# Performance work log

Measured on AMD Instinct MI355X. Metric: run time of the kernel, lower is better.

The kernel has to match this reference:

```python
import jax, jax.numpy as jnp
import numpy as np

HEADS = 4
OUT = 100   # = max_num_peds
IN = 100    # = max_num_peds
NEG_SLOPE = 0.2  # both GATConv attention leakyrelu (PyG default) and module's nn.LeakyReLU(0.2)


def setup_inputs() -> dict:
    key = jax.random.key(0)
    k0, k1, k2, k3 = jax.random.split(key, 4)
    A = jax.random.normal(k0, (1024, 100, 100), jnp.float32)
    # GATConv linear weight [heads*out, in] and attention vectors [heads, out]
    W = jax.random.normal(k1, (HEADS * OUT, IN), jnp.float32) * 0.1
    att_src = jax.random.normal(k2, (HEADS, OUT), jnp.float32) * 0.1
    att_dst = jax.random.normal(k3, (HEADS, OUT), jnp.float32) * 0.1
    bias = jnp.zeros((OUT,), jnp.float32)
    return {"A": A, "W": W, "att_src": att_src, "att_dst": att_dst, "bias": bias}


def reference(A, W, att_src, att_dst, bias):
    # A: [T, N, N] with N == max_num_peds, so the F.pad in the original is a no-op.
    T, _, N = A.shape
    X = jnp.swapaxes(A, 1, 2)                      # x = A_t.T for every t -> [T, N, IN]
    Wh = W.reshape(HEADS, OUT, IN)
    H = jnp.einsum('tnf,hof->tnho', X, Wh)         # per-head projected features [T,N,H,OUT]
    a_s = jnp.einsum('tnho,ho->tnh', H, att_src)   # source attention logits [T,N,H]
    a_d = jnp.einsum('tnho,ho->tnh', H, att_dst)   # dest attention logits   [T,N,H]
    # fully-connected graph + self loops (PyG add_self_loops=True) -> dense [T, i, j, H]
    logits = jax.nn.leaky_relu(a_d[:, :, None, :] + a_s[:, None, :, :], NEG_SLOPE)
    alpha = jax.nn.softmax(logits, axis=2)         # softmax over source nodes j per dest i
    out = jnp.einsum('tijh,tjho->tiho', alpha, H)  # aggregate [T,N,H,OUT]
    out = out.mean(axis=2) + bias                  # concat=False -> mean over heads, + bias
    x = jax.nn.leaky_relu(out, NEG_SLOPE)          # module's self.lrelu
    new_A = jnp.swapaxes(x, 1, 2)[:, :N, :N] + jnp.eye(N, dtype=A.dtype)
    return new_A
```

## Files before the change

### kernel.cpp

```cpp
#include <hip/hip_runtime.h>
#include <hip/hip_bf16.h>

typedef __attribute__((ext_vector_type(8))) short bf16x8;
typedef __attribute__((ext_vector_type(4))) float f32x4;
typedef __attribute__((ext_vector_type(4))) unsigned u32x4;

#define NEG 0.2f
#define CST 104
#define HSTRIDE 11648
#define POFF 24192

__device__ __forceinline__ float lrelu(float x) { return x >= 0.0f ? x : NEG * x; }

__device__ __forceinline__ unsigned pk2(float a, float b) {
    __hip_bfloat162 h = __float22bfloat162_rn(float2{a, b});
    unsigned r;
    __builtin_memcpy(&r, &h, sizeof(r));
    return r;
}
__device__ __forceinline__ float bflo(unsigned u) {
    unsigned v = u << 16; float f; __builtin_memcpy(&f, &v, 4); return f;
}
__device__ __forceinline__ float bfhi(unsigned u) {
    unsigned v = u & 0xffff0000u; float f; __builtin_memcpy(&f, &v, 4); return f;
}

extern "C" __global__ void prep_w(const float* __restrict__ W,
                                  const float* __restrict__ att_src,
                                  const float* __restrict__ att_dst,
                                  unsigned short* __restrict__ Wp)
{
    __shared__ float red[2][4][128];
    __shared__ float sWS[128], sWD[128];
    const int h = blockIdx.x, tid = threadIdx.x;
    const int f = tid & 127, og = tid >> 7;
    const float* __restrict__ Wh = W + h * 10000;
    float ws = 0.0f, wd = 0.0f;
    if (f < 100) {
        for (int o = og * 25; o < og * 25 + 25; ++o) {
            float wv = Wh[o * 100 + f];
            ws = fmaf(att_src[h * 100 + o], wv, ws);
            wd = fmaf(att_dst[h * 100 + o], wv, wd);
        }
    }
    red[0][og][f] = ws;
    red[1][og][f] = wd;
    __syncthreads();
    if (tid < 256) {
        const int which = tid >> 7, ff = tid & 127;
        float s = (red[which][0][ff] + red[which][1][ff]) +
                  (red[which][2][ff] + red[which][3][ff]);
        (which ? sWD : sWS)[ff] = s;
    }
    __syncthreads();
    unsigned short* __restrict__ D = Wp + h * HSTRIDE;
    for (int q = tid; q < 2912; q += 512) {
        const int o = q / 26, f0 = (q - o * 26) * 4;
        uint2 pp = {0u, 0u};
        if (f0 < 100) {
            if (o < 100) {
                float4 wv = *(const float4*)(Wh + o * 100 + f0);
                pp.x = pk2(wv.x, wv.y);
                pp.y = pk2(wv.z, wv.w);
            } else if (o == 100) {
                pp.x = pk2(sWS[f0], sWS[f0 + 1]);
                pp.y = pk2(sWS[f0 + 2], sWS[f0 + 3]);
            } else if (o == 101) {
                pp.x = pk2(sWD[f0], sWD[f0 + 1]);
                pp.y = pk2(sWD[f0 + 2], sWD[f0 + 3]);
            }
        }
        *(uint2*)(D + o * CST + f0) = pp;
    }
}

extern "C" __global__ void __launch_bounds__(512, 4)
gat19(const float* __restrict__ A, const unsigned short* __restrict__ Wp,
      const float* __restrict__ bias, float* __restrict__ out)
{
    extern __shared__ char smem[];
    unsigned short* HT = (unsigned short*)smem;
    float* sas  = (float*)(smem + 23296);
    float* sad  = (float*)(smem + 23744);
    unsigned short* P  = (unsigned short*)(smem + POFF);
    float* sOut = (float*)smem;

    const int t    = blockIdx.x;
    const int tid  = threadIdx.x;
    const int w    = tid >> 6;
    const int l    = tid & 63;
    const int lr   = l & 15;
    const int lk   = l >> 4;
    const bool HASW = (w < 7);
    const int row  = HASW ? w : 6;
    const int j0   = row * 16 + 4 * lk;
    const bool JW  = HASW && (j0 < 104);
    const float* __restrict__ At = A + (size_t)t * 10000u;
    const f32x4 z4 = {0, 0, 0, 0};

    if (tid < 224) {
        float v = (tid >= 100 && tid < 112) ? -1e30f : 0.0f;
        ((float*)(smem + 23296))[tid] = v;
    }

    {
        const char* Wg = (const char*)Wp;
#pragma unroll
        for (int k = 0; k < 3; ++k) {
            const int c0 = k * 512 + w * 64;
            if (c0 < 1456)
                __builtin_amdgcn_global_load_lds(
                    (const __attribute__((address_space(1))) unsigned*)(Wg + c0 * 16 + l * 16),
                    (__attribute__((address_space(3))) unsigned*)(smem + POFF + c0 * 16),
                    16, 0, 0);
        }
    }

    const int col = row * 16 + lr;
    const bool cOK = HASW && (col < 100);
    bf16x8 xf[4];
#pragma unroll
    for (int ks = 0; ks < 4; ++ks) {
        const bool kill = (ks == 3) && (lk != 0);
        const int koff = ks * 32 + lk * 8;
        u32x4 uv = {0u, 0u, 0u, 0u};
        if (cOK && !kill) {
#pragma unroll
            for (int jp = 0; jp < 4; ++jp) {
                const int f0 = koff + jp * 2;
                float a0 = (f0     < 100) ? At[f0 * 100 + col]       : 0.0f;
                float a1 = (f0 + 1 < 100) ? At[(f0 + 1) * 100 + col] : 0.0f;
                uv[jp] = pk2(a0, a1);
            }
        }
        xf[ks] = __builtin_bit_cast(bf16x8, uv);
    }
    __syncthreads();

    f32x4 acc[7];
#pragma unroll
    for (int c = 0; c < 7; ++c) acc[c] = z4;

    for (int h = 0; h < 4; ++h) {
        if (HASW) {
#pragma unroll
            for (int half = 0; half < 2; ++half) {
                const int ntn = half ? 3 : 4;
                f32x4 c[4];
#pragma unroll
                for (int cc = 0; cc < 4; ++cc) c[cc] = z4;
                __builtin_amdgcn_s_setprio(1);
#pragma unroll
                for (int ks = 0; ks < 4; ++ks) {
                    const int koff = ks * 32 + lk * 8;
                    bf16x8 b[4];
#pragma unroll
                    for (int bb = 0; bb < 4; ++bb)
                        if (bb < ntn)
                            b[bb] = *(const bf16x8*)(P + ((half * 4 + bb) * 16 + lr) * CST + koff);
#pragma unroll
                    for (int bb = 0; bb < 4; ++bb)
                        if (bb < ntn)
                            c[bb] = __builtin_amdgcn_mfma_f32_16x16x32_bf16(xf[ks], b[bb], c[bb], 0, 0, 0);
                }
                __builtin_amdgcn_s_setprio(0);
#pragma unroll
                for (int bb = 0; bb < 4; ++bb)
                    if (bb < ntn) {
                        const int o = (half * 4 + bb) * 16 + lr;
                        if (JW) {
                            uint2 pp;
                            pp.x = pk2(c[bb].x, c[bb].y);
                            pp.y = pk2(c[bb].z, c[bb].w);
                            *(uint2*)(HT + o * CST + j0) = pp;
                        }
                    }
                if (half == 1) {
                    if (lr == 4 && j0 < 100) *(f32x4*)(sas + j0) = c[2];
                    if (lr == 5 && JW)       *(f32x4*)(sad + j0) = c[2];
                }
            }
        }
        __syncthreads();

        if (h < 3) {
            const char* Wg = (const char*)(Wp + (h + 1) * HSTRIDE);
#pragma unroll
            for (int k = 0; k < 3; ++k) {
                const int c0 = k * 512 + w * 64;
                if (c0 < 1456)
                    __builtin_amdgcn_global_load_lds(
                        (const __attribute__((address_space(1))) unsigned*)(Wg + c0 * 16 + l * 16),
                        (__attribute__((address_space(3))) unsigned*)(smem + POFF + c0 * 16),
                        16, 0, 0);
            }
        }

        if (HASW) {
            const float adi = sad[row * 16 + lr];
            float sE = 0.0f;
            bf16x8 af[4];
#pragma unroll
            for (int ks = 0; ks < 4; ++ks) {
                const bool dead = (ks == 3) && (lk != 0);
                const int jb = dead ? 64 : ks * 32 + lk * 8;
                const f32x4 s0 = *(const f32x4*)(sas + jb);
                const f32x4 s1 = *(const f32x4*)(sas + jb + 4);
                float e0 = dead ? 0.0f : __expf(lrelu(adi + s0.x));
                float e1 = dead ? 0.0f : __expf(lrelu(adi + s0.y));
                float e2 = dead ? 0.0f : __expf(lrelu(adi + s0.z));
                float e3 = dead ? 0.0f : __expf(lrelu(adi + s0.w));
                float e4 = dead ? 0.0f : __expf(lrelu(adi + s1.x));
                float e5 = dead ? 0.0f : __expf(lrelu(adi + s1.y));
                float e6 = dead ? 0.0f : __expf(lrelu(adi + s1.z));
                float e7 = dead ? 0.0f : __expf(lrelu(adi + s1.w));
                sE += ((e0 + e1) + (e2 + e3)) + ((e4 + e5) + (e6 + e7));
                u32x4 uv;
                uv.x = pk2(e0, e1); uv.y = pk2(e2, e3);
                uv.z = pk2(e4, e5); uv.w = pk2(e6, e7);
                af[ks] = __builtin_bit_cast(bf16x8, uv);
            }
            sE += __shfl_xor(sE, 16);
            sE += __shfl_xor(sE, 32);
            const float invE = sE > 0.0f ? __builtin_amdgcn_rcpf(sE) : 0.0f;
#pragma unroll
            for (int ks = 0; ks < 4; ++ks) {
                u32x4 uv = __builtin_bit_cast(u32x4, af[ks]);
                uv.x = pk2(bflo(uv.x) * invE, bfhi(uv.x) * invE);
                uv.y = pk2(bflo(uv.y) * invE, bfhi(uv.y) * invE);
                uv.z = pk2(bflo(uv.z) * invE, bfhi(uv.z) * invE);
                uv.w = pk2(bflo(uv.w) * invE, bfhi(uv.w) * invE);
                af[ks] = __builtin_bit_cast(bf16x8, uv);
            }

            __builtin_amdgcn_s_setprio(1);
#pragma unroll
            for (int half = 0; half < 2; ++half) {
                const int ntn = half ? 3 : 4;
#pragma unroll
                for (int ks = 0; ks < 4; ++ks) {
                    const int koff = ks * 32 + lk * 8;
                    bf16x8 b[4];
#pragma unroll
                    for (int bb = 0; bb < 4; ++bb)
                        if (bb < ntn)
                            b[bb] = *(const bf16x8*)(HT + ((half * 4 + bb) * 16 + lr) * CST + koff);
#pragma unroll
                    for (int bb = 0; bb < 4; ++bb)
                        if (bb < ntn)
                            acc[half * 4 + bb] = __builtin_amdgcn_mfma_f32_16x16x32_bf16(
                                af[ks], b[bb], acc[half * 4 + bb], 0, 0, 0);
                }
            }
            __builtin_amdgcn_s_setprio(0);
        }
        __syncthreads();
    }

    if (JW) {
        const int i0 = j0;
#pragma unroll
        for (int tn = 0; tn < 7; ++tn) {
            const int o = tn * 16 + lr;
            const float b = (o < 100) ? bias[o] : 0.0f;
            f32x4 v;
            v.x = lrelu(acc[tn].x * 0.25f + b) + ((i0 + 0) == o ? 1.0f : 0.0f);
            v.y = lrelu(acc[tn].y * 0.25f + b) + ((i0 + 1) == o ? 1.0f : 0.0f);
            v.z = lrelu(acc[tn].z * 0.25f + b) + ((i0 + 2) == o ? 1.0f : 0.0f);
            v.w = lrelu(acc[tn].w * 0.25f + b) + ((i0 + 3) == o ? 1.0f : 0.0f);
            *(f32x4*)(sOut + o * 104 + i0) = v;
        }
    }
    __syncthreads();

    float* __restrict__ outT = out + (size_t)t * 10000u;
    for (int q = tid; q < 2500; q += 512) {
        int o = q / 25, i0 = (q - o * 25) * 4;
        *(float4*)(outT + o * 100 + i0) = *(const float4*)(sOut + o * 104 + i0);
    }
}

extern "C" void kernel_launch(void* const* d_in, const int* in_sizes, int n_in,
                              void* d_out, int out_size, void* d_ws, size_t ws_size,
                              hipStream_t stream) {
    const float* A      = (const float*)d_in[0];
    const float* W      = (const float*)d_in[1];
    const float* attsrc = (const float*)d_in[2];
    const float* attdst = (const float*)d_in[3];
    const float* bias   = (const float*)d_in[4];
    float* outp = (float*)d_out;
    unsigned short* Wp = (unsigned short*)d_ws;

    const int T = in_sizes[0] / 10000;

    prep_w<<<4, 512, 0, stream>>>(W, attsrc, attdst, Wp);

    const int smem_bytes = 47744;
    gat19<<<T, 512, smem_bytes, stream>>>(A, Wp, bias, outp);
}
```

Before: 66.33 us.

## Halve block to 4 waves, each computing two 16-row tiles

```diff
diff --git a/kernel.cpp b/kernel.cpp
--- a/kernel.cpp
+++ b/kernel.cpp
@@ -74,8 +74,8 @@
     }
 }
 
-extern "C" __global__ void __launch_bounds__(512, 4)
-gat19(const float* __restrict__ A, const unsigned short* __restrict__ Wp,
+extern "C" __global__ void __launch_bounds__(256, 3)
+gat20(const float* __restrict__ A, const unsigned short* __restrict__ Wp,
       const float* __restrict__ bias, float* __restrict__ out)
 {
     extern __shared__ char smem[];
@@ -91,10 +91,11 @@
     const int l    = tid & 63;
     const int lr   = l & 15;
     const int lk   = l >> 4;
-    const bool HASW = (w < 7);
-    const int row  = HASW ? w : 6;
-    const int j0   = row * 16 + 4 * lk;
-    const bool JW  = HASW && (j0 < 104);
+    const bool HAS2 = (w < 3);
+    const int tr1  = HAS2 ? (w + 4) : w;
+    const int j00  = w * 16 + 4 * lk;
+    const int j01  = tr1 * 16 + 4 * lk;
+    const bool JW1 = HAS2 && (j01 < 104);
     const float* __restrict__ At = A + (size_t)t * 10000u;
     const f32x4 z4 = {0, 0, 0, 0};
 
@@ -102,12 +103,13 @@
         float v = (tid >= 100 && tid < 112) ? -1e30f : 0.0f;
         ((float*)(smem + 23296))[tid] = v;
     }
+    if (tid >= 224 && tid < 240) ((unsigned*)smem)[tid - 224] = 0;
 
     {
         const char* Wg = (const char*)Wp;
 #pragma unroll
-        for (int k = 0; k < 3; ++k) {
-            const int c0 = k * 512 + w * 64;
+        for (int k = 0; k < 6; ++k) {
+            const int c0 = k * 256 + w * 64;
             if (c0 < 1456)
                 __builtin_amdgcn_global_load_lds(
                     (const __attribute__((address_space(1))) unsigned*)(Wg + c0 * 16 + l * 16),
@@ -116,68 +118,88 @@
         }
     }
 
-    const int col = row * 16 + lr;
-    const bool cOK = HASW && (col < 100);
-    bf16x8 xf[4];
+    const int col0 = w * 16 + lr;
+    const int col1 = tr1 * 16 + lr;
+    const bool c1OK = col1 < 100;
+    bf16x8 xf[2][4];
 #pragma unroll
     for (int ks = 0; ks < 4; ++ks) {
         const bool kill = (ks == 3) && (lk != 0);
         const int koff = ks * 32 + lk * 8;
-        u32x4 uv = {0u, 0u, 0u, 0u};
-        if (cOK && !kill) {
+        u32x4 uv0 = {0u, 0u, 0u, 0u}, uv1 = {0u, 0u, 0u, 0u};
+        if (!kill) {
 #pragma unroll
             for (int jp = 0; jp < 4; ++jp) {
                 const int f0 = koff + jp * 2;
-                float a0 = (f0     < 100) ? At[f0 * 100 + col]       : 0.0f;
-                float a1 = (f0 + 1 < 100) ? At[(f0 + 1) * 100 + col] : 0.0f;
-                uv[jp] = pk2(a0, a1);
-            }
-        }
-        xf[ks] = __builtin_bit_cast(bf16x8, uv);
+                const bool g0 = (f0 < 100), g1 = (f0 + 1 < 100);
+                float a0 = g0 ? At[f0 * 100 + col0] : 0.0f;
+                float a1 = g1 ? At[(f0 + 1) * 100 + col0] : 0.0f;
+                uv0[jp] = pk2(a0, a1);
+                float b0 = (g0 && c1OK) ? At[f0 * 100 + col1] : 0.0f;
+                float b1 = (g1 && c1OK) ? At[(f0 + 1) * 100 + col1] : 0.0f;
+                uv1[jp] = pk2(b0, b1);
+            }
+        }
+        xf[0][ks] = __builtin_bit_cast(bf16x8, uv0);
+        xf[1][ks] = __builtin_bit_cast(bf16x8, uv1);
     }
     __syncthreads();
 
-    f32x4 acc[7];
-#pragma unroll
-    for (int c = 0; c < 7; ++c) acc[c] = z4;
+    f32x4 acc[2][7];
+#pragma unroll
+    for (int r = 0; r < 2; ++r)
+#pragma unroll
+        for (int c = 0; c < 7; ++c) acc[r][c] = z4;
 
     for (int h = 0; h < 4; ++h) {
-        if (HASW) {
-#pragma unroll
-            for (int half = 0; half < 2; ++half) {
-                const int ntn = half ? 3 : 4;
-                f32x4 c[4];
-#pragma unroll
-                for (int cc = 0; cc < 4; ++cc) c[cc] = z4;
-                __builtin_amdgcn_s_setprio(1);
-#pragma unroll
-                for (int ks = 0; ks < 4; ++ks) {
-                    const int koff = ks * 32 + lk * 8;
-                    bf16x8 b[4];
-#pragma unroll
-                    for (int bb = 0; bb < 4; ++bb)
-                        if (bb < ntn)
-                            b[bb] = *(const bf16x8*)(P + ((half * 4 + bb) * 16 + lr) * CST + koff);
-#pragma unroll
-                    for (int bb = 0; bb < 4; ++bb)
-                        if (bb < ntn)
-                            c[bb] = __builtin_amdgcn_mfma_f32_16x16x32_bf16(xf[ks], b[bb], c[bb], 0, 0, 0);
-                }
-                __builtin_amdgcn_s_setprio(0);
+#pragma unroll
+        for (int half = 0; half < 2; ++half) {
+            const int ntn = half ? 3 : 4;
+            f32x4 c0[4], c1[4];
+#pragma unroll
+            for (int cc = 0; cc < 4; ++cc) { c0[cc] = z4; c1[cc] = z4; }
+            __builtin_amdgcn_s_setprio(1);
+#pragma unroll
+            for (int ks = 0; ks < 4; ++ks) {
+                const int koff = ks * 32 + lk * 8;
+                bf16x8 b[4];
+#pragma unroll
+                for (int bb = 0; bb < 4; ++bb)
+                    if (bb < ntn)
+                        b[bb] = *(const bf16x8*)(P + ((half * 4 + bb) * 16 + lr) * CST + koff);
 #pragma unroll
                 for (int bb = 0; bb < 4; ++bb)
                     if (bb < ntn) {
-                        const int o = (half * 4 + bb) * 16 + lr;
-                        if (JW) {
-                            uint2 pp;
-                            pp.x = pk2(c[bb].x, c[bb].y);
-                            pp.y = pk2(c[bb].z, c[bb].w);
-                            *(uint2*)(HT + o * CST + j0) = pp;
-                        }
+                        c0[bb] = __builtin_amdgcn_mfma_f32_16x16x32_bf16(xf[0][ks], b[bb], c0[bb], 0, 0, 0);
+                        c1[bb] = __builtin_amdgcn_mfma_f32_16x16x32_bf16(xf[1][ks], b[bb], c1[bb], 0, 0, 0);
                     }
-                if (half == 1) {
-                    if (lr == 4 && j0 < 100) *(f32x4*)(sas + j0) = c[2];
-                    if (lr == 5 && JW)       *(f32x4*)(sad + j0) = c[2];
+            }
+            __builtin_amdgcn_s_setprio(0);
+#pragma unroll
+            for (int bb = 0; bb < 4; ++bb)
+                if (bb < ntn) {
+                    const int o = (half * 4 + bb) * 16 + lr;
+                    {
+                        uint2 pp;
+                        pp.x = pk2(c0[bb].x, c0[bb].y);
+                        pp.y = pk2(c0[bb].z, c0[bb].w);
+                        *(uint2*)(HT + o * CST + j00) = pp;
+                    }
+                    if (JW1) {
+                        uint2 pp;
+                        pp.x = pk2(c1[bb].x, c1[bb].y);
+                        pp.y = pk2(c1[bb].z, c1[bb].w);
+                        *(uint2*)(HT + o * CST + j01) = pp;
+                    }
+                }
+            if (half == 1) {
+                if (lr == 4) {
+                    *(f32x4*)(sas + j00) = c0[2];
+                    if (HAS2 && j01 < 100) *(f32x4*)(sas + j01) = c1[2];
+                }
+                if (lr == 5) {
+                    *(f32x4*)(sad + j00) = c0[2];
+                    if (JW1) *(f32x4*)(sad + j01) = c1[2];
                 }
             }
         }
@@ -186,95 +208,137 @@
         if (h < 3) {
             const char* Wg = (const char*)(Wp + (h + 1) * HSTRIDE);
 #pragma unroll
-            for (int k = 0; k < 3; ++k) {
-                const int c0 = k * 512 + w * 64;
-                if (c0 < 1456)
+            for (int k = 0; k < 6; ++k) {
+                const int c0i = k * 256 + w * 64;
+                if (c0i < 1456)
                     __builtin_amdgcn_global_load_lds(
-                        (const __attribute__((address_space(1))) unsigned*)(Wg + c0 * 16 + l * 16),
-                        (__attribute__((address_space(3))) unsigned*)(smem + POFF + c0 * 16),
+                        (const __attribute__((address_space(1))) unsigned*)(Wg + c0i * 16 + l * 16),
+                        (__attribute__((address_space(3))) unsigned*)(smem + POFF + c0i * 16),
                         16, 0, 0);
             }
         }
 
-        if (HASW) {
-            const float adi = sad[row * 16 + lr];
-            float sE = 0.0f;
-            bf16x8 af[4];
-#pragma unroll
-            for (int ks = 0; ks < 4; ++ks) {
-                const bool dead = (ks == 3) && (lk != 0);
-                const int jb = dead ? 64 : ks * 32 + lk * 8;
-                const f32x4 s0 = *(const f32x4*)(sas + jb);
-                const f32x4 s1 = *(const f32x4*)(sas + jb + 4);
-                float e0 = dead ? 0.0f : __expf(lrelu(adi + s0.x));
-                float e1 = dead ? 0.0f : __expf(lrelu(adi + s0.y));
-                float e2 = dead ? 0.0f : __expf(lrelu(adi + s0.z));
-                float e3 = dead ? 0.0f : __expf(lrelu(adi + s0.w));
-                float e4 = dead ? 0.0f : __expf(lrelu(adi + s1.x));
-                float e5 = dead ? 0.0f : __expf(lrelu(adi + s1.y));
-                float e6 = dead ? 0.0f : __expf(lrelu(adi + s1.z));
-                float e7 = dead ? 0.0f : __expf(lrelu(adi + s1.w));
-                sE += ((e0 + e1) + (e2 + e3)) + ((e4 + e5) + (e6 + e7));
+        const float adi0 = sad[col0];
+        const float adi1 = sad[col1];
+        float sE0 = 0.0f, sE1 = 0.0f;
+        bf16x8 af0[4], af1[4];
+#pragma unroll
+        for (int ks = 0; ks < 4; ++ks) {
+            const bool dead = (ks == 3) && (lk != 0);
+            const int jb = dead ? 64 : ks * 32 + lk * 8;
+            const f32x4 s0 = *(const f32x4*)(sas + jb);
+            const f32x4 s1 = *(const f32x4*)(sas + jb + 4);
+            {
+                float e0 = dead ? 0.0f : __expf(lrelu(adi0 + s0.x));
+                float e1 = dead ? 0.0f : __expf(lrelu(adi0 + s0.y));
+                float e2 = dead ? 0.0f : __expf(lrelu(adi0 + s0.z));
+                float e3 = dead ? 0.0f : __expf(lrelu(adi0 + s0.w));
+                float e4 = dead ? 0.0f : __expf(lrelu(adi0 + s1.x));
+                float e5 = dead ? 0.0f : __expf(lrelu(adi0 + s1.y));
+                float e6 = dead ? 0.0f : __expf(lrelu(adi0 + s1.z));
+                float e7 = dead ? 0.0f : __expf(lrelu(adi0 + s1.w));
+                sE0 += ((e0 + e1) + (e2 + e3)) + ((e4 + e5) + (e6 + e7));
                 u32x4 uv;
                 uv.x = pk2(e0, e1); uv.y = pk2(e2, e3);
                 uv.z = pk2(e4, e5); uv.w = pk2(e6, e7);
-                af[ks] = __builtin_bit_cast(bf16x8, uv);
-            }
-            sE += __shfl_xor(sE, 16);
-            sE += __shfl_xor(sE, 32);
-            const float invE = sE > 0.0f ? __builtin_amdgcn_rcpf(sE) : 0.0f;
+                af0[ks] = __builtin_bit_cast(bf16x8, uv);
+            }
+            {
+                float e0 = dead ? 0.0f : __expf(lrelu(adi1 + s0.x));
+                float e1 = dead ? 0.0f : __expf(lrelu(adi1 + s0.y));
+                float e2 = dead ? 0.0f : __expf(lrelu(adi1 + s0.z));
+                float e3 = dead ? 0.0f : __expf(lrelu(adi1 + s0.w));
+                float e4 = dead ? 0.0f : __expf(lrelu(adi1 + s1.x));
+                float e5 = dead ? 0.0f : __expf(lrelu(adi1 + s1.y));
+                float e6 = dead ? 0.0f : __expf(lrelu(adi1 + s1.z));
+                float e7 = dead ? 0.0f : __expf(lrelu(adi1 + s1.w));
+                sE1 += ((e0 + e1) + (e2 + e3)) + ((e4 + e5) + (e6 + e7));
+                u32x4 uv;
+                uv.x = pk2(e0, e1); uv.y = pk2(e2, e3);
+                uv.z = pk2(e4, e5); uv.w = pk2(e6, e7);
+                af1[ks] = __builtin_bit_cast(bf16x8, uv);
+            }
+        }
+        sE0 += __shfl_xor(sE0, 16);
+        sE0 += __shfl_xor(sE0, 32);
+        sE1 += __shfl_xor(sE1, 16);
+        sE1 += __shfl_xor(sE1, 32);
+        const float invE0 = sE0 > 0.0f ? __builtin_amdgcn_rcpf(sE0) : 0.0f;
+        const float invE1 = sE1 > 0.0f ? __builtin_amdgcn_rcpf(sE1) : 0.0f;
+#pragma unroll
+        for (int ks = 0; ks < 4; ++ks) {
+            u32x4 u0 = __builtin_bit_cast(u32x4, af0[ks]);
+            u0.x = pk2(bflo(u0.x) * invE0, bfhi(u0.x) * invE0);
+            u0.y = pk2(bflo(u0.y) * invE0, bfhi(u0.y) * invE0);
+            u0.z = pk2(bflo(u0.z) * invE0, bfhi(u0.z) * invE0);
+            u0.w = pk2(bflo(u0.w) * invE0, bfhi(u0.w) * invE0);
+            af0[ks] = __builtin_bit_cast(bf16x8, u0);
+            u32x4 u1 = __builtin_bit_cast(u32x4, af1[ks]);
+            u1.x = pk2(bflo(u1.x) * invE1, bfhi(u1.x) * invE1);
+            u1.y = pk2(bflo(u1.y) * invE1, bfhi(u1.y) * invE1);
+            u1.z = pk2(bflo(u1.z) * invE1, bfhi(u1.z) * invE1);
+            u1.w = pk2(bflo(u1.w) * invE1, bfhi(u1.w) * invE1);
+            af1[ks] = __builtin_bit_cast(bf16x8, u1);
+        }
+
+        __builtin_amdgcn_s_setprio(1);
+#pragma unroll
+        for (int half = 0; half < 2; ++half) {
+            const int ntn = half ? 3 : 4;
 #pragma unroll
             for (int ks = 0; ks < 4; ++ks) {
-                u32x4 uv = __builtin_bit_cast(u32x4, af[ks]);
-                uv.x = pk2(bflo(uv.x) * invE, bfhi(uv.x) * invE);
-                uv.y = pk2(bflo(uv.y) * invE, bfhi(uv.y) * invE);
-                uv.z = pk2(bflo(uv.z) * invE, bfhi(uv.z) * invE);
-                uv.w = pk2(bflo(uv.w) * invE, bfhi(uv.w) * invE);
-                af[ks] = __builtin_bit_cast(bf16x8, uv);
-            }
-
-            __builtin_amdgcn_s_setprio(1);
-#pragma unroll
-            for (int half = 0; half < 2; ++half) {
-                const int ntn = half ? 3 : 4;
-#pragma unroll
-                for (int ks = 0; ks < 4; ++ks) {
-                    const int koff = ks * 32 + lk * 8;
-                    bf16x8 b[4];
-#pragma unroll
-                    for (int bb = 0; bb < 4; ++bb)
-                        if (bb < ntn)
-                            b[bb] = *(const bf16x8*)(HT + ((half * 4 + bb) * 16 + lr) * CST + koff);
-#pragma unroll
-                    for (int bb = 0; bb < 4; ++bb)
-                        if (bb < ntn)
-                            acc[half * 4 + bb] = __builtin_amdgcn_mfma_f32_16x16x32_bf16(
-                                af[ks], b[bb], acc[half * 4 + bb], 0, 0, 0);
-                }
-            }
-            __builtin_amdgcn_s_setprio(0);
-        }
+                const int koff = ks * 32 + lk * 8;
+                bf16x8 b[4];
+#pragma unroll
+                for (int bb = 0; bb < 4; ++bb)
+                    if (bb < ntn)
+                        b[bb] = *(const bf16x8*)(HT + ((half * 4 + bb) * 16 + lr) * CST + koff);
+#pragma unroll
+                for (int bb = 0; bb < 4; ++bb)
+                    if (bb < ntn) {
+                        acc[0][half * 4 + bb] = __builtin_amdgcn_mfma_f32_16x16x32_bf16(
+                            af0[ks], b[bb], acc[0][half * 4 + bb], 0, 0, 0);
+                        acc[1][half * 4 + bb] = __builtin_amdgcn_mfma_f32_16x16x32_bf16(
+                            af1[ks], b[bb], acc[1][half * 4 + bb], 0, 0, 0);
+                    }
+            }
+        }
+        __builtin_amdgcn_s_setprio(0);
         __syncthreads();
     }
 
-    if (JW) {
-        const int i0 = j0;
+    {
+        const int i0 = j00;
 #pragma unroll
         for (int tn = 0; tn < 7; ++tn) {
             const int o = tn * 16 + lr;
             const float b = (o < 100) ? bias[o] : 0.0f;
             f32x4 v;
-            v.x = lrelu(acc[tn].x * 0.25f + b) + ((i0 + 0) == o ? 1.0f : 0.0f);
-            v.y = lrelu(acc[tn].y * 0.25f + b) + ((i0 + 1) == o ? 1.0f : 0.0f);
-            v.z = lrelu(acc[tn].z * 0.25f + b) + ((i0 + 2) == o ? 1.0f : 0.0f);
-            v.w = lrelu(acc[tn].w * 0.25f + b) + ((i0 + 3) == o ? 1.0f : 0.0f);
+            v.x = lrelu(acc[0][tn].x * 0.25f + b) + ((i0 + 0) == o ? 1.0f : 0.0f);
+            v.y = lrelu(acc[0][tn].y * 0.25f + b) + ((i0 + 1) == o ? 1.0f : 0.0f);
+            v.z = lrelu(acc[0][tn].z * 0.25f + b) + ((i0 + 2) == o ? 1.0f : 0.0f);
+            v.w = lrelu(acc[0][tn].w * 0.25f + b) + ((i0 + 3) == o ? 1.0f : 0.0f);
             *(f32x4*)(sOut + o * 104 + i0) = v;
         }
     }
+    if (JW1) {
+        const int i0 = j01;
+#pragma unroll
+        for (int tn = 0; tn < 7; ++tn) {
+            const int o = tn * 16 + lr;
+            const float b = (o < 100) ? bias[o] : 0.0f;
+            f32x4 v;
+            v.x = lrelu(acc[1][tn].x * 0.25f + b) + ((i0 + 0) == o ? 1.0f : 0.0f);
+            v.y = lrelu(acc[1][tn].y * 0.25f + b) + ((i0 + 1) == o ? 1.0f : 0.0f);
+            v.z = lrelu(acc[1][tn].z * 0.25f + b) + ((i0 + 2) == o ? 1.0f : 0.0f);
+            v.w = lrelu(acc[1][tn].w * 0.25f + b) + ((i0 + 3) == o ? 1.0f : 0.0f);
+            *(f32x4*)(sOut + o * 104 + i0) = v;
+        }
+    }
     __syncthreads();
 
     float* __restrict__ outT = out + (size_t)t * 10000u;
-    for (int q = tid; q < 2500; q += 512) {
+    for (int q = tid; q < 2500; q += 256) {
         int o = q / 25, i0 = (q - o * 25) * 4;
         *(float4*)(outT + o * 100 + i0) = *(const float4*)(sOut + o * 104 + i0);
     }
@@ -296,5 +360,5 @@
     prep_w<<<4, 512, 0, stream>>>(W, attsrc, attdst, Wp);
 
     const int smem_bytes = 47744;
-    gat19<<<T, 512, smem_bytes, stream>>>(A, Wp, bias, outp);
-}
+    gat20<<<T, 256, smem_bytes, stream>>>(A, Wp, bias, outp);
+}
```

New measurement: 100.6 us. 51.7% more time.
